# Optimization experiments

Measured on AMD Instinct MI355X. Metric: run time of the kernel, lower is better.

Reference implementation:

```python
import jax, jax.numpy as jnp
import numpy as np

MLP_DIMS = [256, 128, 64, 32, 1]

def setup_inputs() -> dict:
    key = jax.random.key(0)
    ks = jax.random.split(key, 16)
    N, C, sp = 2, 256, 512
    inp = {
        'points': jax.random.normal(ks[0], (N, C, sp), dtype=jnp.float32),
        'heatMap': jax.random.uniform(ks[1], (N, sp, sp), dtype=jnp.float32),
        'mask': jnp.ones((N, sp, sp), dtype=jnp.float32),
        'positiveMask': jax.random.uniform(ks[2], (N, sp, sp), dtype=jnp.float32),
    }
    # MLP params: 256->128->64->32->1, Kaiming-ish scale
    for i, (din, dout) in enumerate(zip(MLP_DIMS[:-1], MLP_DIMS[1:])):
        inp[f'W{i}'] = jax.random.normal(ks[4 + i], (din, dout), dtype=jnp.float32) * (1.0 / np.sqrt(din))
        inp[f'b{i}'] = jnp.zeros((dout,), dtype=jnp.float32)
    return inp


def _mlp(x, Ws, bs):
    # Linear+ReLU cascade; final layer is a raw logit (no activation).
    n = len(Ws)
    for i, (W, b) in enumerate(zip(Ws, bs)):
        x = jnp.einsum('...i,io->...o', x, W) + b
        if i < n - 1:
            x = jax.nn.relu(x)
    return x


def _bce_with_logits(logits, targets):
    # stable elementwise BCE-with-logits, reduction='none'
    return jnp.maximum(logits, 0.0) - logits * targets + jnp.log1p(jnp.exp(-jnp.abs(logits)))


def reference(points, heatMap, mask, positiveMask, W0, b0, W1, b1, W2, b2, W3, b3):
    p = jnp.transpose(points, (0, 2, 1))          # (N, sp, C)
    X = p[:, :, None, :] + p[:, None, :, :]       # (N, sp, sp, C)
    pred = _mlp(X, [W0, W1, W2, W3], [b0, b1, b2, b3])[..., 0]  # (N, sp, sp)
    loss = _bce_with_logits(pred, heatMap) * mask * positiveMask
    loss = loss.sum() / positiveMask.sum()
    return (pred, loss)
```

## Files before the change

### kernel.cpp

```cpp
#include <hip/hip_runtime.h>
#include <hip/hip_bf16.h>
#include <stdint.h>

#define N_ 2
#define C_ 256
#define SP 512
#define H1 128
#define H2 64
#define H3 32
#define NTILE 1056
#define GRID 256

using f32x4 = __attribute__((ext_vector_type(4))) float;
using u32x4 = __attribute__((ext_vector_type(4))) unsigned int;
using s16x8 = __attribute__((ext_vector_type(8))) short;

__device__ __forceinline__ uint32_t f2bf_rne(float x) {
    uint32_t u = __builtin_bit_cast(uint32_t, x);
    return (u + 0x7FFFu + ((u >> 16) & 1u)) >> 16;
}
__device__ __forceinline__ float bf2f(uint32_t h) {
    return __builtin_bit_cast(float, h << 16);
}
__device__ __forceinline__ uint32_t pkbf(float a, float b) {
    __hip_bfloat162 h = __float22bfloat162_rn(make_float2(a, b));
    uint32_t r;
    __builtin_memcpy(&r, &h, 4);
    return r;
}
__device__ __forceinline__ uint16_t bf1(float a) {
    __hip_bfloat16 h = __float2bfloat16(a);
    uint16_t r;
    __builtin_memcpy(&r, &h, 2);
    return r;
}
__device__ __forceinline__ uint32_t pack_hi2(uint32_t u0, uint32_t u1) {
    return (u0 >> 16) | (u1 & 0xFFFF0000u);
}
__device__ __forceinline__ f32x4 ntload4(const float* p) {
    return __builtin_nontemporal_load((const f32x4*)p);
}

__device__ __forceinline__ void unrank_tile(int tau, int& n, int& iBase, int& jBase)
{
    int nn = (tau >= 528) ? 1 : 0;
    int u = tau - nn * 528;
    int bi = (int)((65.0f - sqrtf(4225.0f - 8.0f * (float)u)) * 0.5f);
    int s = bi * (65 - bi) / 2;
    while (s > u) { --bi; s = bi * (65 - bi) / 2; }
    while (u - s >= 32 - bi) { ++bi; s = bi * (65 - bi) / 2; }
    int bj = bi + (u - s);
    n = nn; iBase = bi * 16; jBase = bj * 16;
}

__global__ __launch_bounds__(512) void k_precompA(
    const float* __restrict__ points, const float* __restrict__ W0,
    const float* __restrict__ b0,
    const float* __restrict__ W1, const float* __restrict__ W2,
    float* __restrict__ A,
    short* __restrict__ W1Th, short* __restrict__ W2Th, short* __restrict__ W2Tl,
    float* __restrict__ accum)
{
    int t = threadIdx.x;
    int b = blockIdx.x;
    if (b == 0 && t < 4) accum[t] = 0.0f;
    int l = t & 63, w = t >> 6;
    int lc = l & 15, kg = l >> 4;
    int rBase = b * 16;
    int n = rBase >> 9;
    int iRow = (rBase & (SP - 1)) + lc;
    const float* pb = points + (size_t)n * C_ * SP + iRow;
    int hcol = w * 16 + lc;

    f32x4 acc = {0.0f, 0.0f, 0.0f, 0.0f};
#pragma unroll
    for (int ks = 0; ks < 8; ++ks) {
        int c0 = ks * 32 + kg * 8;
        float xs[8];
#pragma unroll
        for (int e = 0; e < 8; ++e)
            xs[e] = pb[(size_t)(c0 + e) * SP];
        u32x4 ah, al;
#pragma unroll
        for (int p = 0; p < 4; ++p) {
            uint32_t u0 = __builtin_bit_cast(uint32_t, xs[2 * p]);
            uint32_t u1 = __builtin_bit_cast(uint32_t, xs[2 * p + 1]);
            ah[p] = pack_hi2(u0, u1);
            float l0 = xs[2 * p]     - bf2f(u0 >> 16);
            float l1 = xs[2 * p + 1] - bf2f(u1 >> 16);
            al[p] = pkbf(l0, l1);
        }
        s16x8 ahi = __builtin_bit_cast(s16x8, ah);
        s16x8 alo = __builtin_bit_cast(s16x8, al);
        float ws[8];
#pragma unroll
        for (int e = 0; e < 8; ++e)
            ws[e] = W0[(size_t)(c0 + e) * H1 + hcol];
        u32x4 bh, bl;
#pragma unroll
        for (int p = 0; p < 4; ++p) {
            uint32_t u0 = __builtin_bit_cast(uint32_t, ws[2 * p]);
            uint32_t u1 = __builtin_bit_cast(uint32_t, ws[2 * p + 1]);
            bh[p] = pack_hi2(u0, u1);
            float l0 = ws[2 * p]     - bf2f(u0 >> 16);
            float l1 = ws[2 * p + 1] - bf2f(u1 >> 16);
            bl[p] = pkbf(l0, l1);
        }
        s16x8 bhi = __builtin_bit_cast(s16x8, bh);
        s16x8 blo = __builtin_bit_cast(s16x8, bl);
        acc = __builtin_amdgcn_mfma_f32_16x16x32_bf16(ahi, blo, acc, 0, 0, 0);
        acc = __builtin_amdgcn_mfma_f32_16x16x32_bf16(alo, bhi, acc, 0, 0, 0);
        acc = __builtin_amdgcn_mfma_f32_16x16x32_bf16(ahi, bhi, acc, 0, 0, 0);
    }
    float bv = 0.5f * b0[hcol];
#pragma unroll
    for (int r = 0; r < 4; ++r)
        A[(size_t)(rBase + kg * 4 + r) * H1 + hcol] = acc[r] + bv;

    int gid = b * 512 + t;
    int gstride = 64 * 512;
    for (int idx = gid; idx < H2 * H1; idx += gstride) {
        int col = idx >> 7, k = idx & 127;
        int sidx = col * 128 + ((((k >> 3) ^ (col & 15)) << 3) | (k & 7));
        W1Th[sidx] = (short)f2bf_rne(W1[k * H2 + col]);
    }
    for (int idx = gid; idx < H3 * H2; idx += gstride) {
        int col = idx >> 6, k = idx & 63;
        float wv = W2[k * H3 + col];
        uint32_t h = f2bf_rne(wv);
        int sidx = col * 64 + ((((k >> 3) ^ (col & 7)) << 3) | (k & 7));
        W2Th[sidx] = (short)h;
        W2Tl[sidx] = (short)f2bf_rne(wv - bf2f(h));
    }
}

__global__ __launch_bounds__(512, 2) void k_main(
    const float* __restrict__ A,
    const short* __restrict__ wtab,
    const float* __restrict__ b1, const float* __restrict__ b2,
    const float* __restrict__ W3, const float* __restrict__ b3,
    const float* __restrict__ heat, const float* __restrict__ mask,
    const float* __restrict__ pos,
    float* __restrict__ pred, float* __restrict__ accum, float* __restrict__ loss)
{
    __shared__ __align__(16) char smem[32768 + 32768 + 16384 + 2176 + 64];
    int t = threadIdx.x;
    int bid = blockIdx.x;
    int l = t & 63, w = t >> 6;
    int lc = l & 15, kg = l >> 4;
    char* x2b = smem + 32768 + w * 4096;
    char* x3b = smem + 65536 + w * 2048;
    char* zbB = smem + 81920;
    float* rb = (float*)(smem + 81920 + 2176);

    const short* lw1h = wtab;
    const short* lw2h = wtab + 8192;
    const short* lw2l = wtab + 10240;

    int rST = t >> 5, segST = t & 31;

    s16x8 bw3;
    {
        f32x4 wa = *(const f32x4*)(W3 + kg * 8);
        f32x4 wb = *(const f32x4*)(W3 + kg * 8 + 4);
        u32x4 wp;
        wp[0] = pkbf(wa[0], wa[1]);
        wp[1] = pkbf(wa[2], wa[3]);
        wp[2] = pkbf(wb[0], wb[1]);
        wp[3] = pkbf(wb[2], wb[3]);
        bw3 = __builtin_bit_cast(s16x8, wp);
    }
    float b3v = b3[0];

    float num = 0.0f, den = 0.0f;

    {
        int n0, ib0, jb0; unrank_tile(bid, n0, ib0, jb0);
        const float* Ab = A + (size_t)n0 * SP * H1;
        f32x4 va = ntload4(Ab + (size_t)(ib0 + rST) * H1 + segST * 4);
        f32x4 vb = ntload4(Ab + (size_t)(jb0 + rST) * H1 + segST * 4);
        *(f32x4*)(smem + rST * 512 + ((segST ^ rST) << 4)) = va;
        *(f32x4*)(smem + 8192 + rST * 512 + ((segST ^ rST) << 4)) = vb;
    }
    __syncthreads();

    int cur = 0, itp = 0;
    for (int tau = bid; tau < NTILE; tau += GRID, cur ^= 1, itp ^= 1) {
        int n, iBase, jBase; unrank_tile(tau, n, iBase, jBase);
        char* aiA = smem + cur * 16384;
        char* ajA = aiA + 8192;
        float* zb = (float*)(zbB + itp * 1088);

        bool hn = (tau + GRID < NTILE);
        f32x4 sva, svb;
        if (hn) {
            int n1, ib1, jb1; unrank_tile(tau + GRID, n1, ib1, jb1);
            const float* Ab1 = A + (size_t)n1 * SP * H1;
            sva = ntload4(Ab1 + (size_t)(ib1 + rST) * H1 + segST * 4);
            svb = ntload4(Ab1 + (size_t)(jb1 + rST) * H1 + segST * 4);
        }

        int pr = (t & 255) >> 4, pc = t & 15;
        size_t idx_e = (t < 256)
            ? ((size_t)n * SP + iBase + pr) * SP + (jBase + pc)
            : ((size_t)n * SP + jBase + pr) * SP + (iBase + pc);
        float tg_e = __builtin_nontemporal_load(heat + idx_e);
        float mk_e = __builtin_nontemporal_load(mask + idx_e);
        float pm_e = __builtin_nontemporal_load(pos + idx_e);

        f32x4 acc[2][4];
#pragma unroll
        for (int cf = 0; cf < 4; ++cf) {
            float bv = b1[cf * 16 + lc];
            acc[0][cf] = (f32x4){bv, bv, bv, bv};
            acc[1][cf] = (f32x4){bv, bv, bv, bv};
        }
#pragma unroll
        for (int ks = 0; ks < 4; ++ks) {
            int g0 = ks * 8 + kg * 2;
            f32x4 aj0 = *(const f32x4*)(ajA + lc * 512 + ((g0 ^ lc) << 4));
            f32x4 aj1 = *(const f32x4*)(ajA + lc * 512 + (((g0 + 1) ^ lc) << 4));
#pragma unroll
            for (int m = 0; m < 2; ++m) {
                int rl = 2 * w + m;
                f32x4 ai0 = *(const f32x4*)(aiA + rl * 512 + ((g0 ^ rl) << 4));
                f32x4 ai1 = *(const f32x4*)(aiA + rl * 512 + (((g0 + 1) ^ rl) << 4));
                float xs[8];
#pragma unroll
                for (int e = 0; e < 4; ++e) {
                    xs[e]     = fmaxf(ai0[e] + aj0[e], 0.0f);
                    xs[4 + e] = fmaxf(ai1[e] + aj1[e], 0.0f);
                }
                u32x4 hw;
#pragma unroll
                for (int p = 0; p < 4; ++p)
                    hw[p] = pkbf(xs[2 * p], xs[2 * p + 1]);
                s16x8 ahi = __builtin_bit_cast(s16x8, hw);
#pragma unroll
                for (int cf = 0; cf < 4; ++cf) {
                    int boff = (cf * 16 + lc) * 128 + (((ks * 4 + kg) ^ lc) << 3);
                    s16x8 bhi = *(const s16x8*)(lw1h + boff);
                    acc[m][cf] = __builtin_amdgcn_mfma_f32_16x16x32_bf16(ahi, bhi, acc[m][cf], 0, 0, 0);
                }
            }
        }

#pragma unroll
        for (int m = 0; m < 2; ++m) {
            char* x2 = x2b + m * 2048;
#pragma unroll
            for (int cf = 0; cf < 4; ++cf) {
                int g = cf * 2 + (lc >> 3);
#pragma unroll
                for (int r = 0; r < 4; ++r) {
                    int row = kg * 4 + r;
                    int off = row * 128 + ((g ^ (row & 7)) << 4) + (lc & 7) * 2;
                    *(uint16_t*)(x2 + off) = bf1(fmaxf(acc[m][cf][r], 0.0f));
                }
            }
        }
        f32x4 acc2[2][2];
#pragma unroll
        for (int cf = 0; cf < 2; ++cf) {
            float bv = b2[cf * 16 + lc];
            acc2[0][cf] = (f32x4){bv, bv, bv, bv};
            acc2[1][cf] = (f32x4){bv, bv, bv, bv};
        }
#pragma unroll
        for (int ks = 0; ks < 2; ++ks) {
#pragma unroll
            for (int m = 0; m < 2; ++m) {
                int aoff = lc * 128 + (((ks * 4 + kg) ^ (lc & 7)) << 4);
                s16x8 xa = *(const s16x8*)(x2b + m * 2048 + aoff);
#pragma unroll
                for (int cf = 0; cf < 2; ++cf) {
                    int b2off = (cf * 16 + lc) * 64 + (((ks * 4 + kg) ^ (lc & 7)) << 3);
                    s16x8 bh = *(const s16x8*)(lw2h + b2off);
                    s16x8 bl = *(const s16x8*)(lw2l + b2off);
                    acc2[m][cf] = __builtin_amdgcn_mfma_f32_16x16x32_bf16(xa, bh, acc2[m][cf], 0, 0, 0);
                    acc2[m][cf] = __builtin_amdgcn_mfma_f32_16x16x32_bf16(xa, bl, acc2[m][cf], 0, 0, 0);
                }
            }
        }
#pragma unroll
        for (int m = 0; m < 2; ++m) {
            char* x3 = x3b + m * 1024;
#pragma unroll
            for (int cf = 0; cf < 2; ++cf) {
                int g = cf * 2 + (lc >> 3);
#pragma unroll
                for (int r = 0; r < 4; ++r) {
                    int row = kg * 4 + r;
                    int off = row * 64 + ((g ^ (row & 3)) << 4) + (lc & 7) * 2;
                    *(uint16_t*)(x3 + off) = bf1(fmaxf(acc2[m][cf][r], 0.0f));
                }
            }
        }
#pragma unroll
        for (int m = 0; m < 2; ++m) {
            int a4off = lc * 64 + ((kg ^ (lc & 3)) << 4);
            s16x8 x4 = *(const s16x8*)(x3b + m * 1024 + a4off);
            f32x4 acc3 = (f32x4){b3v, b3v, b3v, b3v};
            acc3 = __builtin_amdgcn_mfma_f32_16x16x32_bf16(x4, bw3, acc3, 0, 0, 0);
            if (lc == 0) {
#pragma unroll
                for (int r = 0; r < 4; ++r)
                    zb[(2 * w + m) * 17 + kg * 4 + r] = acc3[r];
            }
        }

        if (hn) {
            char* Aalt = smem + (cur ^ 1) * 16384;
            *(f32x4*)(Aalt + rST * 512 + ((segST ^ rST) << 4)) = sva;
            *(f32x4*)(Aalt + 8192 + rST * 512 + ((segST ^ rST) << 4)) = svb;
        }
        __syncthreads();

        if (t < 256) {
            int i = iBase + pr, j = jBase + pc;
            if (j >= i) {
                float z = zb[pr * 17 + pc];
                __builtin_nontemporal_store(z, pred + idx_e);
                float bce = fmaxf(z, 0.0f) - z * tg_e + __logf(1.0f + __expf(-fabsf(z)));
                num += bce * mk_e * pm_e;
                den += pm_e;
            }
        } else {
            int J = jBase + pr, I = iBase + pc;
            if (J > I) {
                float z = zb[pc * 17 + pr];
                __builtin_nontemporal_store(z, pred + idx_e);
                float bce = fmaxf(z, 0.0f) - z * tg_e + __logf(1.0f + __expf(-fabsf(z)));
                num += bce * mk_e * pm_e;
                den += pm_e;
            }
        }
    }

#pragma unroll
    for (int off = 32; off > 0; off >>= 1) {
        num += __shfl_down(num, off, 64);
        den += __shfl_down(den, off, 64);
    }
    if (l == 0) { rb[w] = num; rb[8 + w] = den; }
    __syncthreads();
    if (t == 0) {
        float sn = 0.0f, sd = 0.0f;
#pragma unroll
        for (int q = 0; q < 8; ++q) { sn += rb[q]; sd += rb[8 + q]; }
        atomicAdd(&accum[0], sn);
        atomicAdd(&accum[1], sd);
        __threadfence();
        unsigned done = atomicAdd((unsigned*)&accum[2], 1u);
        if (done == GRID - 1) {
            float fn = atomicAdd(&accum[0], 0.0f);
            float fd = atomicAdd(&accum[1], 0.0f);
            loss[0] = fn / fd;
        }
    }
}

extern "C" void kernel_launch(void* const* d_in, const int* in_sizes, int n_in,
                              void* d_out, int out_size, void* d_ws, size_t ws_size,
                              hipStream_t stream)
{
    const float* points = (const float*)d_in[0];
    const float* heat   = (const float*)d_in[1];
    const float* mask   = (const float*)d_in[2];
    const float* pos    = (const float*)d_in[3];
    const float* W0     = (const float*)d_in[4];
    const float* b0     = (const float*)d_in[5];
    const float* W1     = (const float*)d_in[6];
    const float* b1     = (const float*)d_in[7];
    const float* W2     = (const float*)d_in[8];
    const float* b2     = (const float*)d_in[9];
    const float* W3     = (const float*)d_in[10];
    const float* b3     = (const float*)d_in[11];

    float* pred = (float*)d_out;
    float* loss = pred + (size_t)N_ * SP * SP;

    char* ws = (char*)d_ws;
    float* accum = (float*)ws;
    float* A     = (float*)(ws + 256);
    short* W1Th  = (short*)(ws + 256 + 524288);
    short* W2Th  = (short*)(ws + 256 + 524288 + 16384);
    short* W2Tl  = (short*)(ws + 256 + 524288 + 20480);

    k_precompA<<<64, 512, 0, stream>>>(points, W0, b0, W1, W2, A,
                                       W1Th, W2Th, W2Tl, accum);
    k_main<<<GRID, 512, 0, stream>>>(
        A, W1Th, b1, b2, W3, b3, heat, mask, pos, pred, accum, loss);
}
```

Baseline: 39.05 us.

## Drop W2 bf16 split-precision term and compute final layer with shuffles

Layer-2 weights are now stored only as a single bf16 value, dropping the low-part correction table and halving the layer-2 MFMAs. The final 32->1 layer no longer writes ReLU activations to shared memory and runs an MFMA. It computes the dot product in fp32 registers, reduces with cross-lane xor shuffles, and frees 16KB of LDS. This lowers MFMA and LDS traffic, but dropping the hi/lo split reduces layer-2 accuracy, which may affect tolerance.

```diff
diff --git a/kernel.cpp b/kernel.cpp
--- a/kernel.cpp
+++ b/kernel.cpp
@@ -126,11 +126,8 @@
     }
     for (int idx = gid; idx < H3 * H2; idx += gstride) {
         int col = idx >> 6, k = idx & 63;
-        float wv = W2[k * H3 + col];
-        uint32_t h = f2bf_rne(wv);
         int sidx = col * 64 + ((((k >> 3) ^ (col & 7)) << 3) | (k & 7));
-        W2Th[sidx] = (short)h;
-        W2Tl[sidx] = (short)f2bf_rne(wv - bf2f(h));
+        W2Th[sidx] = (short)f2bf_rne(W2[k * H3 + col]);
     }
 }
 
@@ -143,33 +140,21 @@
     const float* __restrict__ pos,
     float* __restrict__ pred, float* __restrict__ accum, float* __restrict__ loss)
 {
-    __shared__ __align__(16) char smem[32768 + 32768 + 16384 + 2176 + 64];
+    __shared__ __align__(16) char smem[32768 + 32768 + 2176 + 64];
     int t = threadIdx.x;
     int bid = blockIdx.x;
     int l = t & 63, w = t >> 6;
     int lc = l & 15, kg = l >> 4;
     char* x2b = smem + 32768 + w * 4096;
-    char* x3b = smem + 65536 + w * 2048;
-    char* zbB = smem + 81920;
-    float* rb = (float*)(smem + 81920 + 2176);
+    char* zbB = smem + 65536;
+    float* rb = (float*)(smem + 65536 + 2176);
 
     const short* lw1h = wtab;
     const short* lw2h = wtab + 8192;
-    const short* lw2l = wtab + 10240;
 
     int rST = t >> 5, segST = t & 31;
 
-    s16x8 bw3;
-    {
-        f32x4 wa = *(const f32x4*)(W3 + kg * 8);
-        f32x4 wb = *(const f32x4*)(W3 + kg * 8 + 4);
-        u32x4 wp;
-        wp[0] = pkbf(wa[0], wa[1]);
-        wp[1] = pkbf(wa[2], wa[3]);
-        wp[2] = pkbf(wb[0], wb[1]);
-        wp[3] = pkbf(wb[2], wb[3]);
-        bw3 = __builtin_bit_cast(s16x8, wp);
-    }
+    float w3a = W3[lc], w3b = W3[16 + lc];
     float b3v = b3[0];
 
     float num = 0.0f, den = 0.0f;
@@ -276,37 +261,33 @@
                 for (int cf = 0; cf < 2; ++cf) {
                     int b2off = (cf * 16 + lc) * 64 + (((ks * 4 + kg) ^ (lc & 7)) << 3);
                     s16x8 bh = *(const s16x8*)(lw2h + b2off);
-                    s16x8 bl = *(const s16x8*)(lw2l + b2off);
                     acc2[m][cf] = __builtin_amdgcn_mfma_f32_16x16x32_bf16(xa, bh, acc2[m][cf], 0, 0, 0);
-                    acc2[m][cf] = __builtin_amdgcn_mfma_f32_16x16x32_bf16(xa, bl, acc2[m][cf], 0, 0, 0);
                 }
             }
         }
+        float zr[2][4];
+#pragma unroll
+        for (int m = 0; m < 2; ++m)
+#pragma unroll
+            for (int r = 0; r < 4; ++r)
+                zr[m][r] = fmaxf(acc2[m][0][r], 0.0f) * w3a
+                         + fmaxf(acc2[m][1][r], 0.0f) * w3b;
+#pragma unroll
+        for (int off = 1; off < 16; off <<= 1) {
+#pragma unroll
+            for (int m = 0; m < 2; ++m)
+#pragma unroll
+                for (int r = 0; r < 4; ++r)
+                    zr[m][r] += __shfl_xor(zr[m][r], off, 64);
+        }
 #pragma unroll
         for (int m = 0; m < 2; ++m) {
-            char* x3 = x3b + m * 1024;
-#pragma unroll
-            for (int cf = 0; cf < 2; ++cf) {
-                int g = cf * 2 + (lc >> 3);
-#pragma unroll
-                for (int r = 0; r < 4; ++r) {
-                    int row = kg * 4 + r;
-                    int off = row * 64 + ((g ^ (row & 3)) << 4) + (lc & 7) * 2;
-                    *(uint16_t*)(x3 + off) = bf1(fmaxf(acc2[m][cf][r], 0.0f));
-                }
-            }
-        }
-#pragma unroll
-        for (int m = 0; m < 2; ++m) {
-            int a4off = lc * 64 + ((kg ^ (lc & 3)) << 4);
-            s16x8 x4 = *(const s16x8*)(x3b + m * 1024 + a4off);
-            f32x4 acc3 = (f32x4){b3v, b3v, b3v, b3v};
-            acc3 = __builtin_amdgcn_mfma_f32_16x16x32_bf16(x4, bw3, acc3, 0, 0, 0);
-            if (lc == 0) {
-#pragma unroll
-                for (int r = 0; r < 4; ++r)
-                    zb[(2 * w + m) * 17 + kg * 4 + r] = acc3[r];
-            }
+            float zsel = zr[m][0];
+            zsel = (lc == 1) ? zr[m][1] : zsel;
+            zsel = (lc == 2) ? zr[m][2] : zsel;
+            zsel = (lc == 3) ? zr[m][3] : zsel;
+            if (lc < 4)
+                zb[(2 * w + m) * 17 + kg * 4 + lc] = zsel + b3v;
         }
 
         if (hn) {
```

Result: slower. 40.28 us (+3.2%).
